# Kernel tuning notes

Hardware: AMD Instinct MI355X
Metric: run time of the kernel (lower is better)

Reference implementation:

```python
import jax, jax.numpy as jnp
import numpy as np

N_NODES = 50000
N_EDGES = 800000
N_GRAPHS = 256
IN_CH = 128
HID = 256
FFN = 256
OUT = 1


def xavier(key, shape):
    fan_in, fan_out = shape[0], shape[1]
    a = jnp.sqrt(6.0 / (fan_in + fan_out))
    return jax.random.uniform(key, shape, jnp.float32, -a, a)


def setup_inputs() -> dict:
    key = jax.random.key(0)
    ks = jax.random.split(key, 12)
    x = jax.random.normal(ks[0], (N_NODES, IN_CH), jnp.float32)
    edge_index = jax.random.randint(ks[1], (2, N_EDGES), 0, N_NODES, jnp.int32)
    batch = jnp.sort(jax.random.randint(ks[2], (N_NODES,), 0, N_GRAPHS, jnp.int32))
    return {
        "x": x,
        "edge_index": edge_index,
        "batch": batch,
        # GCNConv layers (glorot weight, zero bias as in PyG reset_parameters)
        "W1": xavier(ks[3], (IN_CH, HID)), "b1": jnp.zeros((HID,), jnp.float32),
        "W2": xavier(ks[4], (HID, HID)),   "b2": jnp.zeros((HID,), jnp.float32),
        "W3": xavier(ks[5], (HID, HID)),   "b3": jnp.zeros((HID,), jnp.float32),
        # FFN: Linear(HID, FFN) then final Linear(FFN, OUT)
        "Wf": xavier(ks[6], (HID, FFN)),   "bf": jnp.zeros((FFN,), jnp.float32),
        "Wo": xavier(ks[7], (FFN, OUT)),   "bo": jnp.zeros((OUT,), jnp.float32),
    }


def _gcn_norm(edge_index, n_nodes):
    # add self-loops, compute symmetric normalization D^-1/2 (A+I) D^-1/2
    loops = jnp.arange(n_nodes, dtype=edge_index.dtype)
    row = jnp.concatenate([edge_index[0], loops])
    col = jnp.concatenate([edge_index[1], loops])
    deg = jax.ops.segment_sum(jnp.ones_like(col, jnp.float32), col, num_segments=n_nodes)
    dis = jnp.where(deg > 0, jax.lax.rsqrt(jnp.maximum(deg, 1.0)), 0.0)
    norm = dis[row] * dis[col]  # [E+N]
    return row, col, norm


def _gcn_conv(x, W, b, row, col, norm, n_nodes):
    xw = x @ W                                   # [N, H]
    msg = xw[row] * norm[:, None]                # gather + scale  [E+N, H]
    out = jax.ops.segment_sum(msg, col, num_segments=n_nodes)
    return out + b


def reference(x, edge_index, batch, W1, b1, W2, b2, W3, b3, Wf, bf, Wo, bo):
    row, col, norm = _gcn_norm(edge_index, N_NODES)
    h = jax.nn.relu(_gcn_conv(x, W1, b1, row, col, norm, N_NODES))
    h = jax.nn.relu(_gcn_conv(h, W2, b2, row, col, norm, N_NODES))
    h = jax.nn.relu(_gcn_conv(h, W3, b3, row, col, norm, N_NODES))
    # global mean pool over graphs
    counts = jax.ops.segment_sum(jnp.ones((N_NODES,), jnp.float32), batch, num_segments=N_GRAPHS)
    pooled = jax.ops.segment_sum(h, batch, num_segments=N_GRAPHS) / jnp.maximum(counts, 1.0)[:, None]
    # FFN (dropout is identity in eval mode): Linear -> ReLU -> final Linear
    g = jax.nn.relu(pooled @ Wf + bf)
    out = g @ Wo + bo
    return out
```

## Files before the change

### kernel.cpp

```cpp
#include <hip/hip_runtime.h>
#include <hip/hip_bf16.h>
#include <hip/hip_fp16.h>


#define THREADS 256

typedef _Float16 f16x8 __attribute__((ext_vector_type(8)));
typedef float    f32x4 __attribute__((ext_vector_type(4)));


__global__ void degree_goff_kernel(const int* __restrict__ col, int* __restrict__ deg, int E,
                                   const int* __restrict__ batch, int* __restrict__ goff,
                                   int N, int G) {
    int i = blockIdx.x * THREADS + threadIdx.x;
    if (i < E) atomicAdd(&deg[col[i]], 1);
    if (i < N) {
        int b1 = batch[i];
        int b0 = (i == 0) ? -1 : batch[i - 1];
        for (int g = b0 + 1; g <= b1; ++g) goff[g] = i;
        if (i == N - 1) {
            for (int g = b1 + 1; g <= G; ++g) goff[g] = N;
        }
    }
}

__global__ __launch_bounds__(256) void scanA_kernel(
    const int* __restrict__ in, int* __restrict__ out, int* __restrict__ bsum,
    float* __restrict__ dis, int n) {
    __shared__ int wsum[4];
    int i0 = blockIdx.x * 1024 + threadIdx.x * 4;
    int lane = threadIdx.x & 63, wid = threadIdx.x >> 6;
    int v0 = 0, v1 = 0, v2 = 0, v3 = 0;
    if (i0 + 3 < n) {
        int4 v = *(const int4*)&in[i0];
        v0 = v.x; v1 = v.y; v2 = v.z; v3 = v.w;
    } else {
        if (i0 + 0 < n) v0 = in[i0 + 0];
        if (i0 + 1 < n) v1 = in[i0 + 1];
        if (i0 + 2 < n) v2 = in[i0 + 2];
        if (i0 + 3 < n) v3 = in[i0 + 3];
    }
    if (i0 + 0 < n) dis[i0 + 0] = rsqrtf((float)(v0 + 1));
    if (i0 + 1 < n) dis[i0 + 1] = rsqrtf((float)(v1 + 1));
    if (i0 + 2 < n) dis[i0 + 2] = rsqrtf((float)(v2 + 1));
    if (i0 + 3 < n) dis[i0 + 3] = rsqrtf((float)(v3 + 1));
    int s = v0 + v1 + v2 + v3;
    int inc = s;
    #pragma unroll
    for (int d = 1; d < 64; d <<= 1) {
        int t = __shfl_up(inc, d);
        if (lane >= d) inc += t;
    }
    if (lane == 63) wsum[wid] = inc;
    __syncthreads();
    int add = 0;
    for (int w = 0; w < wid; ++w) add += wsum[w];
    int ex = add + inc - s;
    if (i0 + 0 < n) out[i0 + 0] = ex;
    if (i0 + 1 < n) out[i0 + 1] = ex + v0;
    if (i0 + 2 < n) out[i0 + 2] = ex + v0 + v1;
    if (i0 + 3 < n) out[i0 + 3] = ex + v0 + v1 + v2;
    if (threadIdx.x == 255) bsum[blockIdx.x] = add + inc;
}

__global__ void scanB_kernel(int* __restrict__ bsum, int* __restrict__ total_slot, int nb) {
    int lane = threadIdx.x;
    int v = (lane < nb) ? bsum[lane] : 0;
    int inc = v;
    #pragma unroll
    for (int d = 1; d < 64; d <<= 1) {
        int t = __shfl_up(inc, d);
        if (lane >= d) inc += t;
    }
    if (lane < nb) bsum[lane] = inc - v;
    if (lane == 63) *total_slot = inc;
}

__global__ void csr_fill_kernel(const int* __restrict__ row, const int* __restrict__ col,
                                const int* __restrict__ offs, int* __restrict__ deg,
                                int* __restrict__ srcs, int E) {
    int e = blockIdx.x * THREADS + threadIdx.x;
    if (e < E) {
        int c = col[e];
        int old = atomicSub(&deg[c], 1);
        srcs[offs[c] + old - 1] = row[e];
    }
}

__global__ void convert_kernel(
    int* __restrict__ offs, const int* __restrict__ bsum, int Nfix,
    const float* __restrict__ X, const float* __restrict__ dis,
    _Float16* __restrict__ Xs, int total8, int IC,
    const float* __restrict__ W1, _Float16* __restrict__ W1t, int k1,
    const float* __restrict__ W2, _Float16* __restrict__ W2t,
    const float* __restrict__ W3, _Float16* __restrict__ W3t) {
    int i = blockIdx.x * THREADS + threadIdx.x;
    if (i < Nfix) {
        offs[i] += bsum[i >> 10];
        return;
    }
    int j = i - Nfix;
    if (j < total8) {
        int idx = j * 8;
        float d = dis[idx / IC];
        float4 a = *(const float4*)&X[idx];
        float4 b = *(const float4*)&X[idx + 4];
        f16x8 o;
        o[0] = (_Float16)(d * a.x); o[1] = (_Float16)(d * a.y);
        o[2] = (_Float16)(d * a.z); o[3] = (_Float16)(d * a.w);
        o[4] = (_Float16)(d * b.x); o[5] = (_Float16)(d * b.y);
        o[6] = (_Float16)(d * b.z); o[7] = (_Float16)(d * b.w);
        *(f16x8*)&Xs[idx] = o;
        return;
    }
    j -= total8;
    int n1 = k1 * 256;
    if (j < n1) {
        int k = j >> 8, n = j & 255;
        W1t[n * k1 + k] = (_Float16)W1[j];
        return;
    }
    j -= n1;
    if (j < 65536) {
        int k = j >> 8, n = j & 255;
        W2t[n * 256 + k] = (_Float16)W2[j];
        return;
    }
    j -= 65536;
    if (j < 65536) {
        int k = j >> 8, n = j & 255;
        W3t[n * 256 + k] = (_Float16)W3[j];
    }
}


template<int LPN>
__global__ __launch_bounds__(256) void aggregate_f16_kernel(
    const _Float16* __restrict__ X, const int* __restrict__ offs,
    const int* __restrict__ srcs, const float* __restrict__ dis,
    _Float16* __restrict__ A, int N) {
    constexpr int NPB = 256 / LPN;
    int node = blockIdx.x * NPB + threadIdx.x / LPN;
    if (node >= N) return;
    int lane = threadIdx.x % LPN;
    const f16x8* Xv = (const f16x8*)X;
    f16x8 self = Xv[(size_t)node * LPN + lane];
    float acc[8], acc2[8];
    #pragma unroll
    for (int j = 0; j < 8; ++j) { acc[j] = (float)self[j]; acc2[j] = 0.f; }
    int s = offs[node], e = offs[node + 1];
    int i = s;
    for (; i + 4 <= e; i += 4) {
        int s0 = srcs[i], s1 = srcs[i + 1], s2 = srcs[i + 2], s3 = srcs[i + 3];
        f16x8 v0 = Xv[(size_t)s0 * LPN + lane];
        f16x8 v1 = Xv[(size_t)s1 * LPN + lane];
        f16x8 v2 = Xv[(size_t)s2 * LPN + lane];
        f16x8 v3 = Xv[(size_t)s3 * LPN + lane];
        #pragma unroll
        for (int j = 0; j < 8; ++j) {
            acc[j]  += (float)v0[j] + (float)v2[j];
            acc2[j] += (float)v1[j] + (float)v3[j];
        }
    }
    for (; i < e; ++i) {
        int s0 = srcs[i];
        f16x8 v0 = Xv[(size_t)s0 * LPN + lane];
        #pragma unroll
        for (int j = 0; j < 8; ++j) acc[j] += (float)v0[j];
    }
    float dn = dis[node];
    f16x8 o;
    #pragma unroll
    for (int j = 0; j < 8; ++j) o[j] = (_Float16)(dn * (acc[j] + acc2[j]));
    ((f16x8*)A)[(size_t)node * LPN + lane] = o;
}


template<int K, int MODE>
__global__ __launch_bounds__(256) void gemm_as_kernel(
    const _Float16* __restrict__ A, const _Float16* __restrict__ Bt,
    const float* __restrict__ bias, const float* __restrict__ dscale,
    _Float16* __restrict__ H, float* __restrict__ pooled,
    const int* __restrict__ batch, int M) {
    constexpr int LSA = K + 40;
    constexpr int KC = K / 32;
    constexpr int SPR = K / 8;
    __shared__ _Float16 As[64 * LSA];
    int tid = threadIdx.x;
    int m0 = blockIdx.x * 64;

    {
        constexpr int RPI = 256 / SPR;
        int r_in = tid % RPI;
        int seg  = tid / RPI;
        #pragma unroll
        for (int it = 0; it < 64 / RPI; ++it) {
            int r = it * RPI + r_in;
            int gr = m0 + r;
            uint4 v = make_uint4(0, 0, 0, 0);
            if (gr < M) v = *(const uint4*)&A[(size_t)gr * K + seg * 8];
            *(uint4*)&As[r * LSA + seg * 8] = v;
        }
    }
    __syncthreads();

    int wid = tid >> 6, lane = tid & 63;
    int l16 = lane & 15, quad = lane >> 4;
    int wn = wid * 64;

    f32x4 acc[4][4] = {};
    const _Float16* Bbase = Bt + (size_t)(wn + l16) * K + quad * 8;

    #pragma unroll
    for (int kc = 0; kc < KC; ++kc) {
        f16x8 bh[4];
        #pragma unroll
        for (int ni = 0; ni < 4; ++ni)
            bh[ni] = *(const f16x8*)&Bbase[(size_t)(ni * 16) * K + kc * 32];
        #pragma unroll
        for (int mi = 0; mi < 4; ++mi) {
            f16x8 ah = *(const f16x8*)&As[(mi * 16 + l16) * LSA + kc * 32 + quad * 8];
            #pragma unroll
            for (int ni = 0; ni < 4; ++ni)
                acc[mi][ni] = __builtin_amdgcn_mfma_f32_16x16x32_f16(ah, bh[ni], acc[mi][ni], 0, 0, 0);
        }
    }

    #pragma unroll
    for (int mi = 0; mi < 4; ++mi) {
        int rbase = m0 + mi * 16;
        int g0 = 0, g15 = 0;
        if (MODE == 2) {
            g0  = batch[min(rbase, M - 1)];
            g15 = batch[min(rbase + 15, M - 1)];
        }
        #pragma unroll
        for (int ni = 0; ni < 4; ++ni) {
            int col = wn + ni * 16 + l16;
            float bv = bias[col];
            if (MODE == 1) {
                #pragma unroll
                for (int r = 0; r < 4; ++r) {
                    int grow = rbase + quad * 4 + r;
                    if (grow < M) {
                        float v = fmaxf(acc[mi][ni][r] + bv, 0.f) * dscale[grow];
                        H[(size_t)grow * 256 + col] = (_Float16)v;
                    }
                }
            } else {
                if (g0 == g15) {
                    float p = 0.f;
                    #pragma unroll
                    for (int r = 0; r < 4; ++r) {
                        int grow = rbase + quad * 4 + r;
                        float v = fmaxf(acc[mi][ni][r] + bv, 0.f);
                        p += (grow < M) ? v : 0.f;
                    }
                    p += __shfl_xor(p, 16);
                    p += __shfl_xor(p, 32);
                    if (quad == 0) atomicAdd(&pooled[g0 * 256 + col], p);
                } else {
                    #pragma unroll
                    for (int r = 0; r < 4; ++r) {
                        int grow = rbase + quad * 4 + r;
                        if (grow < M) {
                            float v = fmaxf(acc[mi][ni][r] + bv, 0.f);
                            atomicAdd(&pooled[batch[grow] * 256 + col], v);
                        }
                    }
                }
            }
        }
    }
}


__global__ __launch_bounds__(256) void ffn_kernel(
    const float* __restrict__ pooled, const int* __restrict__ goff,
    const float* __restrict__ Wf, const float* __restrict__ bf,
    const float* __restrict__ Wo, const float* __restrict__ bo,
    float* __restrict__ out) {
    __shared__ float p[256];
    __shared__ float red[256];
    int g = blockIdx.x, t = threadIdx.x;
    int cnt = goff[g + 1] - goff[g];
    float inv = 1.f / (float)max(cnt, 1);
    p[t] = pooled[g * 256 + t] * inv;
    __syncthreads();
    float s = bf[t];
    #pragma unroll 8
    for (int k = 0; k < 256; ++k) s = fmaf(p[k], Wf[k * 256 + t], s);
    float gv = fmaxf(s, 0.f);
    red[t] = gv * Wo[t];
    __syncthreads();
    for (int o = 128; o > 0; o >>= 1) {
        if (t < o) red[t] += red[t + o];
        __syncthreads();
    }
    if (t == 0) out[g] = red[0] + bo[0];
}


extern "C" void kernel_launch(void* const* d_in, const int* in_sizes, int n_in,
                              void* d_out, int out_size, void* d_ws, size_t ws_size,
                              hipStream_t stream) {
    const float* x   = (const float*)d_in[0];
    const int*   ei  = (const int*)d_in[1];
    const int*   bat = (const int*)d_in[2];
    const float* W1  = (const float*)d_in[3];
    const float* b1  = (const float*)d_in[4];
    const float* W2  = (const float*)d_in[5];
    const float* b2  = (const float*)d_in[6];
    const float* W3  = (const float*)d_in[7];
    const float* b3  = (const float*)d_in[8];
    const float* Wf  = (const float*)d_in[9];
    const float* bf  = (const float*)d_in[10];
    const float* Wo  = (const float*)d_in[11];
    const float* bo  = (const float*)d_in[12];
    float* out = (float*)d_out;

    const int N  = in_sizes[2];
    const int E  = in_sizes[1] / 2;
    const int IC = in_sizes[0] / N;
    const int HID = 256;
    const int G  = out_size;
    const int* row = ei;
    const int* col = ei + E;

    char* w = (char*)d_ws;
    size_t off = 0;
    auto alloc = [&](size_t bytes) -> void* {
        void* p = w + off;
        off += (bytes + 255) & ~(size_t)255;
        return p;
    };
    int*   deg    = (int*)alloc((size_t)N * 4);
    float* pooled = (float*)alloc((size_t)G * HID * 4);
    float* dis    = (float*)alloc((size_t)N * 4);
    int*   offs   = (int*)alloc((size_t)(N + 1) * 4);
    int*   srcs   = (int*)alloc((size_t)E * 4);
    int*   goff   = (int*)alloc((size_t)(G + 1) * 4);
    int*   bsum   = (int*)alloc((size_t)64 * 4);
    _Float16* W1t = (_Float16*)alloc((size_t)HID * IC * 2);
    _Float16* W2t = (_Float16*)alloc((size_t)HID * HID * 2);
    _Float16* W3t = (_Float16*)alloc((size_t)HID * HID * 2);
    _Float16* Xs  = (_Float16*)alloc((size_t)N * IC * 2);
    _Float16* Ah  = (_Float16*)alloc((size_t)N * HID * 2);
    _Float16* Hs  = (_Float16*)alloc((size_t)N * HID * 2);
    (void)ws_size; (void)n_in;

    size_t zlen = (((size_t)N * 4 + 255) & ~(size_t)255) + (size_t)G * HID * 4;
    hipMemsetAsync(deg, 0, zlen, stream);

    int nb = (N + 1023) / 1024;
    degree_goff_kernel<<<(E + THREADS - 1) / THREADS, THREADS, 0, stream>>>(
        col, deg, E, bat, goff, N, G);
    scanA_kernel<<<nb, 256, 0, stream>>>(deg, offs, bsum, dis, N);
    scanB_kernel<<<1, 64, 0, stream>>>(bsum, &offs[N], nb);

    int total8 = N * IC / 8;
    int conv_total = N + total8 + IC * HID + HID * HID + HID * HID;
    convert_kernel<<<(conv_total + THREADS - 1) / THREADS, THREADS, 0, stream>>>(
        offs, bsum, N, x, dis, Xs, total8, IC, W1, W1t, IC, W2, W2t, W3, W3t);

    csr_fill_kernel<<<(E + THREADS - 1) / THREADS, THREADS, 0, stream>>>(row, col, offs, deg, srcs, E);

    int mtiles = (N + 63) / 64;
    aggregate_f16_kernel<16><<<(N + 15) / 16, 256, 0, stream>>>(Xs, offs, srcs, dis, Ah, N);
    gemm_as_kernel<128, 1><<<mtiles, 256, 0, stream>>>(Ah, W1t, b1, dis, Hs, nullptr, nullptr, N);
    aggregate_f16_kernel<32><<<(N + 7) / 8, 256, 0, stream>>>(Hs, offs, srcs, dis, Ah, N);
    gemm_as_kernel<256, 1><<<mtiles, 256, 0, stream>>>(Ah, W2t, b2, dis, Hs, nullptr, nullptr, N);
    aggregate_f16_kernel<32><<<(N + 7) / 8, 256, 0, stream>>>(Hs, offs, srcs, dis, Ah, N);
    gemm_as_kernel<256, 2><<<mtiles, 256, 0, stream>>>(Ah, W3t, b3, nullptr, nullptr, pooled, bat, N);

    ffn_kernel<<<G, 256, 0, stream>>>(pooled, goff, Wf, bf, Wo, bo, out);
}
```

Measured before the change: 422.1 us.

## Slice features by channel per XCD and store 16-bit CSR indices

Node features and aggregation outputs are stored as eight contiguous channel slices instead of row-major, and aggregation blocks are numbered so that `bid & 7` picks the slice. With round-robin block dispatch, each XCD then gathers from only one slice, roughly 3.2 MB, which should mostly fit in its L2 and cut random-gather traffic to HBM. The GEMM loads and the layer-1/2 epilogue stores are rewritten to match the sliced layout. Source indices are narrowed to unsigned short, and index loads and aggregate stores become nontemporal. The 16-bit indices only work while N is below 65536.

```diff
diff --git a/kernel.cpp b/kernel.cpp
--- a/kernel.cpp
+++ b/kernel.cpp
@@ -78,12 +78,12 @@
 
 __global__ void csr_fill_kernel(const int* __restrict__ row, const int* __restrict__ col,
                                 const int* __restrict__ offs, int* __restrict__ deg,
-                                int* __restrict__ srcs, int E) {
+                                unsigned short* __restrict__ srcs, int E) {
     int e = blockIdx.x * THREADS + threadIdx.x;
     if (e < E) {
         int c = col[e];
         int old = atomicSub(&deg[c], 1);
-        srcs[offs[c] + old - 1] = row[e];
+        srcs[offs[c] + old - 1] = (unsigned short)row[e];
     }
 }
 
@@ -102,7 +102,9 @@
     int j = i - Nfix;
     if (j < total8) {
         int idx = j * 8;
-        float d = dis[idx / IC];
+        int node = idx / IC;
+        int ch0  = idx % IC;
+        float d = dis[node];
         float4 a = *(const float4*)&X[idx];
         float4 b = *(const float4*)&X[idx + 4];
         f16x8 o;
@@ -110,7 +112,9 @@
         o[2] = (_Float16)(d * a.z); o[3] = (_Float16)(d * a.w);
         o[4] = (_Float16)(d * b.x); o[5] = (_Float16)(d * b.y);
         o[6] = (_Float16)(d * b.z); o[7] = (_Float16)(d * b.w);
-        *(f16x8*)&Xs[idx] = o;
+        int sw = IC >> 3;
+        int slice = ch0 / sw, within = ch0 % sw;
+        *(f16x8*)&Xs[((size_t)slice * Nfix + node) * sw + within] = o;
         return;
     }
     j -= total8;
@@ -134,16 +138,20 @@
 }
 
 
-template<int LPN>
-__global__ __launch_bounds__(256) void aggregate_f16_kernel(
+template<int CH>
+__global__ __launch_bounds__(256) void aggregate_slice_kernel(
     const _Float16* __restrict__ X, const int* __restrict__ offs,
-    const int* __restrict__ srcs, const float* __restrict__ dis,
+    const unsigned short* __restrict__ srcs, const float* __restrict__ dis,
     _Float16* __restrict__ A, int N) {
+    constexpr int LPN = CH / 64;
     constexpr int NPB = 256 / LPN;
-    int node = blockIdx.x * NPB + threadIdx.x / LPN;
+    int bid   = blockIdx.x;
+    int slice = bid & 7;
+    int tile  = bid >> 3;
+    int node  = tile * NPB + threadIdx.x / LPN;
     if (node >= N) return;
     int lane = threadIdx.x % LPN;
-    const f16x8* Xv = (const f16x8*)X;
+    const f16x8* Xv = (const f16x8*)X + (size_t)slice * N * LPN;
     f16x8 self = Xv[(size_t)node * LPN + lane];
     float acc[8], acc2[8];
     #pragma unroll
@@ -151,7 +159,10 @@
     int s = offs[node], e = offs[node + 1];
     int i = s;
     for (; i + 4 <= e; i += 4) {
-        int s0 = srcs[i], s1 = srcs[i + 1], s2 = srcs[i + 2], s3 = srcs[i + 3];
+        int s0 = (int)__builtin_nontemporal_load(&srcs[i]);
+        int s1 = (int)__builtin_nontemporal_load(&srcs[i + 1]);
+        int s2 = (int)__builtin_nontemporal_load(&srcs[i + 2]);
+        int s3 = (int)__builtin_nontemporal_load(&srcs[i + 3]);
         f16x8 v0 = Xv[(size_t)s0 * LPN + lane];
         f16x8 v1 = Xv[(size_t)s1 * LPN + lane];
         f16x8 v2 = Xv[(size_t)s2 * LPN + lane];
@@ -163,7 +174,7 @@
         }
     }
     for (; i < e; ++i) {
-        int s0 = srcs[i];
+        int s0 = (int)__builtin_nontemporal_load(&srcs[i]);
         f16x8 v0 = Xv[(size_t)s0 * LPN + lane];
         #pragma unroll
         for (int j = 0; j < 8; ++j) acc[j] += (float)v0[j];
@@ -172,7 +183,8 @@
     f16x8 o;
     #pragma unroll
     for (int j = 0; j < 8; ++j) o[j] = (_Float16)(dn * (acc[j] + acc2[j]));
-    ((f16x8*)A)[(size_t)node * LPN + lane] = o;
+    f16x8* Av = (f16x8*)A + (size_t)slice * N * LPN;
+    __builtin_nontemporal_store(o, &Av[(size_t)node * LPN + lane]);
 }
 
 
@@ -185,6 +197,8 @@
     constexpr int LSA = K + 40;
     constexpr int KC = K / 32;
     constexpr int SPR = K / 8;
+    constexpr int SPS = K / 64;
+    constexpr int SW  = K / 8;
     __shared__ _Float16 As[64 * LSA];
     int tid = threadIdx.x;
     int m0 = blockIdx.x * 64;
@@ -193,12 +207,13 @@
         constexpr int RPI = 256 / SPR;
         int r_in = tid % RPI;
         int seg  = tid / RPI;
+        int slice = seg / SPS, sub = seg % SPS;
         #pragma unroll
         for (int it = 0; it < 64 / RPI; ++it) {
             int r = it * RPI + r_in;
             int gr = m0 + r;
             uint4 v = make_uint4(0, 0, 0, 0);
-            if (gr < M) v = *(const uint4*)&A[(size_t)gr * K + seg * 8];
+            if (gr < M) v = *(const uint4*)&A[((size_t)slice * M + gr) * SW + sub * 8];
             *(uint4*)&As[r * LSA + seg * 8] = v;
         }
     }
@@ -239,12 +254,13 @@
             int col = wn + ni * 16 + l16;
             float bv = bias[col];
             if (MODE == 1) {
+                size_t hbase = ((size_t)(col >> 5) * M) * 32 + (col & 31);
                 #pragma unroll
                 for (int r = 0; r < 4; ++r) {
                     int grow = rbase + quad * 4 + r;
                     if (grow < M) {
                         float v = fmaxf(acc[mi][ni][r] + bv, 0.f) * dscale[grow];
-                        H[(size_t)grow * 256 + col] = (_Float16)v;
+                        H[hbase + (size_t)grow * 32] = (_Float16)v;
                     }
                 }
             } else {
@@ -338,7 +354,7 @@
     float* pooled = (float*)alloc((size_t)G * HID * 4);
     float* dis    = (float*)alloc((size_t)N * 4);
     int*   offs   = (int*)alloc((size_t)(N + 1) * 4);
-    int*   srcs   = (int*)alloc((size_t)E * 4);
+    unsigned short* srcs = (unsigned short*)alloc((size_t)E * 2);
     int*   goff   = (int*)alloc((size_t)(G + 1) * 4);
     int*   bsum   = (int*)alloc((size_t)64 * 4);
     _Float16* W1t = (_Float16*)alloc((size_t)HID * IC * 2);
@@ -366,11 +382,13 @@
     csr_fill_kernel<<<(E + THREADS - 1) / THREADS, THREADS, 0, stream>>>(row, col, offs, deg, srcs, E);
 
     int mtiles = (N + 63) / 64;
-    aggregate_f16_kernel<16><<<(N + 15) / 16, 256, 0, stream>>>(Xs, offs, srcs, dis, Ah, N);
+    int nt1 = (N + 127) / 128;
+    aggregate_slice_kernel<128><<<nt1 * 8, 256, 0, stream>>>(Xs, offs, srcs, dis, Ah, N);
     gemm_as_kernel<128, 1><<<mtiles, 256, 0, stream>>>(Ah, W1t, b1, dis, Hs, nullptr, nullptr, N);
-    aggregate_f16_kernel<32><<<(N + 7) / 8, 256, 0, stream>>>(Hs, offs, srcs, dis, Ah, N);
+    int nt2 = (N + 63) / 64;
+    aggregate_slice_kernel<256><<<nt2 * 8, 256, 0, stream>>>(Hs, offs, srcs, dis, Ah, N);
     gemm_as_kernel<256, 1><<<mtiles, 256, 0, stream>>>(Ah, W2t, b2, dis, Hs, nullptr, nullptr, N);
-    aggregate_f16_kernel<32><<<(N + 7) / 8, 256, 0, stream>>>(Hs, offs, srcs, dis, Ah, N);
+    aggregate_slice_kernel<256><<<nt2 * 8, 256, 0, stream>>>(Hs, offs, srcs, dis, Ah, N);
     gemm_as_kernel<256, 2><<<mtiles, 256, 0, stream>>>(Ah, W3t, b3, nullptr, nullptr, pooled, bat, N);
 
     ffn_kernel<<<G, 256, 0, stream>>>(pooled, goff, Wf, bf, Wo, bo, out);
```

After: 458.4 us. 1.09x slower.
